# Performance work log

Hardware: AMD Instinct MI355X
Metric: run time of the kernel (lower is better)

Reference implementation:

```python
import jax, jax.numpy as jnp
import numpy as np

B, S, D_MODEL = 2, 2048, 2048
H, HKV, HD = 16, 16, 128


def setup_inputs() -> dict:
    key = jax.random.key(0)
    k1, k2, k3, k4, k5 = jax.random.split(key, 5)
    hidden_states = jax.random.normal(k1, (B, S, D_MODEL), dtype=jnp.float32)
    cos = jax.random.uniform(k2, (S, HD), dtype=jnp.float32)
    sin = jax.random.uniform(k3, (S, HD), dtype=jnp.float32)
    W_qkv = jax.random.normal(k4, (D_MODEL, (H + 2 * HKV) * HD), dtype=jnp.float32) * (D_MODEL ** -0.5)
    W_o = jax.random.normal(k5, (H * HD, D_MODEL), dtype=jnp.float32) * ((H * HD) ** -0.5)
    return {"hidden_states": hidden_states, "cos": cos, "sin": sin, "W_qkv": W_qkv, "W_o": W_o}


def _rotate_half(x):
    x1, x2 = jnp.split(x, 2, axis=-1)
    return jnp.concatenate([-x2, x1], axis=-1)


def reference(hidden_states, cos, sin, W_qkv, W_o):
    b, s, _ = hidden_states.shape
    qkv = jnp.einsum('bsd,de->bse', hidden_states, W_qkv)
    qkv = qkv.reshape(b, s, H + 2 * HKV, HD)  # B S (H+2Hkv) D
    q = qkv[:, :, :H]
    k = qkv[:, :, H:H + HKV]
    v = qkv[:, :, H + HKV:]
    # rotary: cos/sin [S, D] broadcast over batch and heads
    c = cos[None, :, None, :]
    sn = sin[None, :, None, :]
    q = q * c + _rotate_half(q) * sn
    k = k * c + _rotate_half(k) * sn
    # B S H D -> B H S D
    q = jnp.transpose(q, (0, 2, 1, 3))
    k = jnp.transpose(k, (0, 2, 1, 3))
    v = jnp.transpose(v, (0, 2, 1, 3))
    scale = HD ** -0.5
    scores = jnp.einsum('bhqd,bhkd->bhqk', q, k) * scale
    attn = jax.nn.softmax(scores.astype(jnp.float32), axis=-1).astype(q.dtype)
    attn = jax.lax.stop_gradient(attn)  # frozen attention pattern (detach)
    out = jnp.einsum('bhqk,bhkd->bhqd', attn, v)
    out = jnp.transpose(out, (0, 2, 1, 3)).reshape(b, s, H * HD)
    return jnp.einsum('bsd,de->bse', out, W_o)
```

## Files before the change

kernel.cpp:

```cpp
#include <hip/hip_runtime.h>

typedef _Float16 f16;
typedef _Float16 half8 __attribute__((ext_vector_type(8)));
typedef _Float16 half4 __attribute__((ext_vector_type(4)));
typedef float f32x4 __attribute__((ext_vector_type(4)));

#define B_ 2
#define S_ 2048
#define DM_ 2048
#define H_ 16
#define HD_ 128
#define EQ_ 6144
#define SCALE_Q 0.08838834764831845f
#define DEFER_THR 8.0f

__device__ __forceinline__ void gload16(const void* g, void* l) {
  __builtin_amdgcn_global_load_lds(
      (const __attribute__((address_space(1))) unsigned int*)g,
      (__attribute__((address_space(3))) unsigned int*)l, 16, 0, 0);
}

__device__ __forceinline__ float red16_max(float x) {
  float t;
  t = __builtin_bit_cast(float, __builtin_amdgcn_mov_dpp(__builtin_bit_cast(int, x), 0xB1, 0xF, 0xF, true));
  x = fmaxf(x, t);
  t = __builtin_bit_cast(float, __builtin_amdgcn_mov_dpp(__builtin_bit_cast(int, x), 0x4E, 0xF, 0xF, true));
  x = fmaxf(x, t);
  t = __builtin_bit_cast(float, __builtin_amdgcn_mov_dpp(__builtin_bit_cast(int, x), 0x141, 0xF, 0xF, true));
  x = fmaxf(x, t);
  t = __builtin_bit_cast(float, __builtin_amdgcn_mov_dpp(__builtin_bit_cast(int, x), 0x140, 0xF, 0xF, true));
  x = fmaxf(x, t);
  return x;
}
__device__ __forceinline__ float red16_sum(float x) {
  float t;
  t = __builtin_bit_cast(float, __builtin_amdgcn_mov_dpp(__builtin_bit_cast(int, x), 0xB1, 0xF, 0xF, true));
  x += t;
  t = __builtin_bit_cast(float, __builtin_amdgcn_mov_dpp(__builtin_bit_cast(int, x), 0x4E, 0xF, 0xF, true));
  x += t;
  t = __builtin_bit_cast(float, __builtin_amdgcn_mov_dpp(__builtin_bit_cast(int, x), 0x141, 0xF, 0xF, true));
  x += t;
  t = __builtin_bit_cast(float, __builtin_amdgcn_mov_dpp(__builtin_bit_cast(int, x), 0x140, 0xF, 0xF, true));
  x += t;
  return x;
}

__global__ void k_cast(const float* __restrict__ in, f16* __restrict__ out, int n4) {
  int i = blockIdx.x * blockDim.x + threadIdx.x;
  int stride = gridDim.x * blockDim.x;
  for (; i < n4; i += stride) {
    float4 v = ((const float4*)in)[i];
    half4 h = { (f16)v.x, (f16)v.y, (f16)v.z, (f16)v.w };
    ((half4*)out)[i] = h;
  }
}

__global__ void k_tcast(const float* __restrict__ in, f16* __restrict__ out, int K, int N) {
  __shared__ float tile[64][65];
  const int t = threadIdx.x;
  const int nb = blockIdx.x * 64, kb = blockIdx.y * 64;
  const int tr = t >> 4, tc4 = (t & 15) * 4;
  #pragma unroll
  for (int i = 0; i < 4; ++i) {
    int k = tr + i * 16;
    float4 v = *(const float4*)&in[(size_t)(kb + k) * N + nb + tc4];
    tile[k][tc4 + 0] = v.x; tile[k][tc4 + 1] = v.y;
    tile[k][tc4 + 2] = v.z; tile[k][tc4 + 3] = v.w;
  }
  __syncthreads();
  #pragma unroll
  for (int i = 0; i < 4; ++i) {
    int n = tr + i * 16;
    half4 h = { (f16)tile[tc4 + 0][n], (f16)tile[tc4 + 1][n],
                (f16)tile[tc4 + 2][n], (f16)tile[tc4 + 3][n] };
    *(half4*)&out[(size_t)(nb + n) * K + kb + tc4] = h;
  }
}

__global__ __launch_bounds__(256, 2) void k_gemm(
    const f16* __restrict__ A, const f16* __restrict__ Bt,
    f16* __restrict__ C16, float* __restrict__ C32,
    int M, int N, int K, int writeF32)
{
  __shared__ __attribute__((aligned(16))) f16 As[2 * 128 * 64];
  __shared__ __attribute__((aligned(16))) f16 Bs[2 * 128 * 64];
  const int t = threadIdx.x;
  const int lane = t & 63, wave = t >> 6;
  const int lr = lane & 15, hi4 = lane >> 4;
  const int wr = wave >> 1, wc = wave & 1;
  const int row0 = blockIdx.x * 128, col0 = blockIdx.y * 128;

  const int srow = lane >> 3, schunk = lane & 7;
  const f16* gA = &A[(size_t)(row0 + wave * 32 + srow) * K + ((schunk ^ srow) * 8)];
  const f16* gB = &Bt[(size_t)(col0 + wave * 32 + srow) * K + ((schunk ^ srow) * 8)];
  char* asb = (char*)As;
  char* bsb = (char*)Bs;

  f32x4 acc[4][4];
  #pragma unroll
  for (int m = 0; m < 4; ++m)
    #pragma unroll
    for (int n = 0; n < 4; ++n)
      acc[m][n] = (f32x4){0.f, 0.f, 0.f, 0.f};

  const int nk = K >> 6;
  #pragma unroll
  for (int i = 0; i < 4; ++i) {
    gload16(gA + (size_t)(i * 8) * K, asb + wave * 4096 + i * 1024);
    gload16(gB + (size_t)(i * 8) * K, bsb + wave * 4096 + i * 1024);
  }
  __syncthreads();

  int cur = 0;
  for (int kt = 0; kt < nk; ++kt) {
    if (kt + 1 < nk) {
      int nb = cur ^ 1;
      #pragma unroll
      for (int i = 0; i < 4; ++i) {
        gload16(gA + (size_t)(i * 8) * K + (kt + 1) * 64, asb + nb * 16384 + wave * 4096 + i * 1024);
        gload16(gB + (size_t)(i * 8) * K + (kt + 1) * 64, bsb + nb * 16384 + wave * 4096 + i * 1024);
      }
    }
    const char* ab = asb + cur * 16384;
    const char* bb = bsb + cur * 16384;
    #pragma unroll
    for (int ks = 0; ks < 2; ++ks) {
      half8 af[4], bf[4];
      #pragma unroll
      for (int m = 0; m < 4; ++m) {
        int ar = wr * 64 + m * 16 + lr;
        af[m] = *(const half8*)(ab + ar * 128 + (((ks * 4 + hi4) ^ (ar & 7)) << 4));
      }
      #pragma unroll
      for (int n = 0; n < 4; ++n) {
        int br = wc * 64 + n * 16 + lr;
        bf[n] = *(const half8*)(bb + br * 128 + (((ks * 4 + hi4) ^ (br & 7)) << 4));
      }
      #pragma unroll
      for (int m = 0; m < 4; ++m)
        #pragma unroll
        for (int n = 0; n < 4; ++n)
          acc[m][n] = __builtin_amdgcn_mfma_f32_16x16x32_f16(af[m], bf[n], acc[m][n], 0, 0, 0);
    }
    __syncthreads();
    cur ^= 1;
  }
  #pragma unroll
  for (int m = 0; m < 4; ++m)
    #pragma unroll
    for (int n = 0; n < 4; ++n)
      #pragma unroll
      for (int j = 0; j < 4; ++j) {
        int row = row0 + wr * 64 + m * 16 + hi4 * 4 + j;
        int col = col0 + wc * 64 + n * 16 + lr;
        if (writeF32) C32[(size_t)row * N + col] = acc[m][n][j];
        else          C16[(size_t)row * N + col] = (f16)acc[m][n][j];
      }
  (void)M;
}

__global__ void k_rope(const f16* __restrict__ qkv, const float* __restrict__ cosb,
                       const float* __restrict__ sinb, f16* __restrict__ Qf, f16* __restrict__ Kf)
{
  const int bx = blockIdx.x;
  const int bs = bx >> 4;
  const int h = (bx & 15) * 2 + (threadIdx.x >> 7);
  const int d = threadIdx.x & 127;
  const int s = bs & (S_ - 1);
  const int b = bs >> 11;
  float x  = (float)qkv[(size_t)bs * EQ_ + h * HD_ + d];
  float xp = (float)qkv[(size_t)bs * EQ_ + h * HD_ + (d ^ 64)];
  float sgn = (d < 64) ? -1.0f : 1.0f;
  float v = x * cosb[s * HD_ + d] + sgn * xp * sinb[s * HD_ + d];
  if (h < H_) {
    v *= SCALE_Q;
    Qf[(((size_t)(b * H_ + h)) * S_ + s) * HD_ + d] = (f16)v;
  } else {
    Kf[(((size_t)(b * H_ + (h - H_))) * S_ + s) * HD_ + d] = (f16)v;
  }
}

__global__ void k_vtrans(const f16* __restrict__ qkv, f16* __restrict__ VT)
{
  __shared__ __attribute__((aligned(16))) f16 tile[128][136];
  const int bx = blockIdx.x;
  const int st = bx & 15, h = (bx >> 4) & 15, b = bx >> 8;
  const int t = threadIdx.x;
  const int sl = t >> 1, dc = (t & 1) * 64;
  const int bs = b * S_ + st * 128 + sl;
  #pragma unroll
  for (int i = 0; i < 8; ++i) {
    half8 v = *(const half8*)&qkv[(size_t)bs * EQ_ + (32 + h) * HD_ + dc + i * 8];
    *(half8*)&tile[sl][dc + i * 8] = v;
  }
  __syncthreads();
  const int dr = t >> 1, scc = (t & 1) * 64;
  #pragma unroll
  for (int i = 0; i < 8; ++i) {
    half8 v;
    #pragma unroll
    for (int j = 0; j < 8; ++j) v[j] = tile[scc + i * 8 + j][dr];
    *(half8*)&VT[(((size_t)(b * H_ + h)) * HD_ + dr) * S_ + st * 128 + scc + i * 8] = v;
  }
}

__global__ __launch_bounds__(256, 2) void k_attn(
    const f16* __restrict__ Qf, const f16* __restrict__ Kf, const f16* __restrict__ VT,
    f16* __restrict__ Oout)
{
  __shared__ __attribute__((aligned(16))) char lds[32768];
  char* Ks = lds;
  char* Vs = lds + 16384;
  const int bx = blockIdx.x;
  const int hg = bx & 31, qt = bx >> 5;
  const int h = hg & 15, b = hg >> 4;
  const int t = threadIdx.x, lane = t & 63, wave = t >> 6;
  const int lr = lane & 15, hi4 = lane >> 4;
  char* Ps = Ks + wave * 4096;
  const size_t bh = (size_t)(b * H_ + h);
  const int q0 = qt * 128 + wave * 32;

  half8 qf[2][4];
  #pragma unroll
  for (int m = 0; m < 2; ++m)
    #pragma unroll
    for (int ds = 0; ds < 4; ++ds)
      qf[m][ds] = *(const half8*)&Qf[(bh * S_ + q0 + m * 16 + lr) * HD_ + ds * 32 + hi4 * 8];

  f32x4 o[2][8];
  #pragma unroll
  for (int m = 0; m < 2; ++m)
    #pragma unroll
    for (int dc = 0; dc < 8; ++dc) o[m][dc] = (f32x4){0.f, 0.f, 0.f, 0.f};
  float mstate[2][4], lstate[2][4];
  #pragma unroll
  for (int m = 0; m < 2; ++m)
    #pragma unroll
    for (int j = 0; j < 4; ++j) { mstate[m][j] = -1e30f; lstate[m][j] = 0.f; }

  const f16* Kg = &Kf[bh * S_ * HD_];
  const f16* Vg = &VT[bh * HD_ * S_];

  for (int kt = 0; kt < S_ / 64; ++kt) {
    __syncthreads();
    #pragma unroll
    for (int i = 0; i < 4; ++i) {
      int row = wave * 16 + i * 4 + (lane >> 4);
      int ch  = (lane & 15) ^ (row & 7);
      gload16(Kg + (size_t)(kt * 64 + row) * HD_ + ch * 8, Ks + wave * 4096 + i * 1024);
    }
    #pragma unroll
    for (int i = 0; i < 4; ++i) {
      int d  = wave * 32 + i * 8 + (lane >> 3);
      int ch = (lane & 7) ^ (d & 7);
      gload16(Vg + (size_t)d * S_ + kt * 64 + ch * 8, Vs + wave * 4096 + i * 1024);
    }
    asm volatile("s_waitcnt vmcnt(4)" ::: "memory");
    __builtin_amdgcn_s_barrier();
    __builtin_amdgcn_sched_barrier(0);

    f32x4 sc[2][4];
    #pragma unroll
    for (int m = 0; m < 2; ++m)
      #pragma unroll
      for (int n = 0; n < 4; ++n) sc[m][n] = (f32x4){0.f, 0.f, 0.f, 0.f};
    #pragma unroll
    for (int ds = 0; ds < 4; ++ds) {
      half8 kf[4];
      #pragma unroll
      for (int n = 0; n < 4; ++n) {
        int ar = n * 16 + lr;
        kf[n] = *(const half8*)(Ks + ar * 256 + ((((ds * 4 + hi4) ^ (ar & 7))) << 4));
      }
      #pragma unroll
      for (int m = 0; m < 2; ++m)
        #pragma unroll
        for (int n = 0; n < 4; ++n)
          sc[m][n] = __builtin_amdgcn_mfma_f32_16x16x32_f16(qf[m][ds], kf[n], sc[m][n], 0, 0, 0);
    }
    __syncthreads();

    float mx[2][4];
    #pragma unroll
    for (int m = 0; m < 2; ++m)
      #pragma unroll
      for (int j = 0; j < 4; ++j) {
        mx[m][j] = fmaxf(fmaxf(sc[m][0][j], sc[m][1][j]), fmaxf(sc[m][2][j], sc[m][3][j]));
        mx[m][j] = red16_max(mx[m][j]);
      }
    float dmax = -1e30f;
    #pragma unroll
    for (int m = 0; m < 2; ++m)
      #pragma unroll
      for (int j = 0; j < 4; ++j)
        dmax = fmaxf(dmax, mx[m][j] - mstate[m][j]);
    if (__any(dmax > DEFER_THR)) {
      #pragma unroll
      for (int m = 0; m < 2; ++m)
        #pragma unroll
        for (int j = 0; j < 4; ++j) {
          float nm = fmaxf(mstate[m][j], mx[m][j]);
          float corr = __expf(mstate[m][j] - nm);
          mstate[m][j] = nm;
          lstate[m][j] *= corr;
          #pragma unroll
          for (int dc = 0; dc < 8; ++dc) o[m][dc][j] *= corr;
        }
    }
    float rs[2][4];
    #pragma unroll
    for (int m = 0; m < 2; ++m)
      #pragma unroll
      for (int j = 0; j < 4; ++j) rs[m][j] = 0.f;
    #pragma unroll
    for (int m = 0; m < 2; ++m)
      #pragma unroll
      for (int n = 0; n < 4; ++n)
        #pragma unroll
        for (int j = 0; j < 4; ++j) {
          float p = __expf(sc[m][n][j] - mstate[m][j]);
          sc[m][n][j] = p;
          rs[m][j] += p;
        }
    #pragma unroll
    for (int m = 0; m < 2; ++m)
      #pragma unroll
      for (int j = 0; j < 4; ++j)
        lstate[m][j] += red16_sum(rs[m][j]);

    #pragma unroll
    for (int m = 0; m < 2; ++m)
      #pragma unroll
      for (int n = 0; n < 4; ++n)
        #pragma unroll
        for (int j = 0; j < 4; ++j) {
          int prow = m * 16 + hi4 * 4 + j;
          *(f16*)(Ps + prow * 128 + ((n * 32 + lr * 2) ^ ((prow & 7) << 4))) = (f16)sc[m][n][j];
        }
    asm volatile("" ::: "memory");

    #pragma unroll
    for (int ks = 0; ks < 2; ++ks) {
      half8 pa[2];
      #pragma unroll
      for (int m = 0; m < 2; ++m) {
        int pr = m * 16 + lr;
        pa[m] = *(const half8*)(Ps + pr * 128 + ((((ks * 4 + hi4) ^ (pr & 7))) << 4));
      }
      #pragma unroll
      for (int dc = 0; dc < 8; ++dc) {
        int rv = dc * 16 + lr;
        half8 vb = *(const half8*)(Vs + rv * 128 + ((((ks * 4 + hi4) ^ (rv & 7))) << 4));
        #pragma unroll
        for (int m = 0; m < 2; ++m)
          o[m][dc] = __builtin_amdgcn_mfma_f32_16x16x32_f16(pa[m], vb, o[m][dc], 0, 0, 0);
      }
    }
  }

  float inv[2][4];
  #pragma unroll
  for (int m = 0; m < 2; ++m)
    #pragma unroll
    for (int j = 0; j < 4; ++j) inv[m][j] = 1.0f / lstate[m][j];
  #pragma unroll
  for (int m = 0; m < 2; ++m)
    #pragma unroll
    for (int dc = 0; dc < 8; ++dc)
      #pragma unroll
      for (int j = 0; j < 4; ++j) {
        int row = b * S_ + qt * 128 + wave * 32 + m * 16 + hi4 * 4 + j;
        int col = h * 128 + dc * 16 + lr;
        Oout[(size_t)row * DM_ + col] = (f16)(o[m][dc][j] * inv[m][j]);
      }
}

extern "C" void kernel_launch(void* const* d_in, const int* in_sizes, int n_in,
                              void* d_out, int out_size, void* d_ws, size_t ws_size,
                              hipStream_t stream) {
  (void)in_sizes; (void)n_in; (void)out_size; (void)ws_size;
  const float* hidden = (const float*)d_in[0];
  const float* cosb   = (const float*)d_in[1];
  const float* sinb   = (const float*)d_in[2];
  const float* W_qkv  = (const float*)d_in[3];
  const float* W_o    = (const float*)d_in[4];
  float* out = (float*)d_out;

  f16* Ah    = (f16*)d_ws;
  f16* Wqt   = Ah    + (size_t)8388608;
  f16* Wot   = Wqt   + (size_t)12582912;
  f16* qkv16 = Wot   + (size_t)4194304;
  f16* Qf    = qkv16 + (size_t)25165824;
  f16* Kf    = Qf    + (size_t)8388608;
  f16* VT    = Kf    + (size_t)8388608;
  f16* AO    = VT    + (size_t)8388608;

  k_cast<<<2048, 256, 0, stream>>>(hidden, Ah, 2097152);
  k_tcast<<<dim3(EQ_ / 64, 2048 / 64), 256, 0, stream>>>(W_qkv, Wqt, 2048, EQ_);
  k_tcast<<<dim3(2048 / 64, 2048 / 64), 256, 0, stream>>>(W_o, Wot, 2048, 2048);
  k_gemm<<<dim3(32, EQ_ / 128), 256, 0, stream>>>(Ah, Wqt, qkv16, nullptr, 4096, EQ_, 2048, 0);
  k_rope<<<B_ * S_ * 16, 256, 0, stream>>>(qkv16, cosb, sinb, Qf, Kf);
  k_vtrans<<<512, 256, 0, stream>>>(qkv16, VT);
  k_attn<<<512, 256, 0, stream>>>(Qf, Kf, VT, AO);
  k_gemm<<<dim3(32, 16), 256, 0, stream>>>(AO, Wot, nullptr, out, 4096, 2048, 2048, 1);
}
```

Before: 433.9 us.

## Use 256x256-tile GEMM for QKV projection and vectorize RoPE kernel

Adds a 512-thread GEMM kernel with 256x256 output tiles and double-buffered LDS staging, used for the QKV projection. Each wave computes a 128x64 sub-tile, which raises operand reuse and arithmetic intensity per LDS byte. The grid shrinks to 384 blocks, which may underfill the GPU's CUs and uses more registers. RoPE is also rewritten so each thread processes 8 element pairs with half8 and float4 vector loads, replacing scalar per-element loads.

```diff
diff --git a/kernel.cpp b/kernel.cpp
--- a/kernel.cpp
+++ b/kernel.cpp
@@ -75,6 +75,83 @@
                 (f16)tile[tc4 + 2][n], (f16)tile[tc4 + 3][n] };
     *(half4*)&out[(size_t)(nb + n) * K + kb + tc4] = h;
   }
+}
+
+__global__ __launch_bounds__(512, 2) void k_gemm256(
+    const f16* __restrict__ A, const f16* __restrict__ Bt, f16* __restrict__ C,
+    int N, int K)
+{
+  __shared__ __attribute__((aligned(16))) f16 As[2][256 * 64];
+  __shared__ __attribute__((aligned(16))) f16 Bs[2][256 * 64];
+  const int t = threadIdx.x;
+  const int lane = t & 63, wave = t >> 6;
+  const int lr = lane & 15, hi4 = lane >> 4;
+  const int wm = wave >> 2, wn = wave & 3;
+  const int row0 = blockIdx.x * 256, col0 = blockIdx.y * 256;
+
+  const int srow = lane >> 3, schunk = lane & 7;
+  const f16* gA = &A[(size_t)(row0 + wave * 32 + srow) * K + ((schunk ^ srow) * 8)];
+  const f16* gB = &Bt[(size_t)(col0 + wave * 32 + srow) * K + ((schunk ^ srow) * 8)];
+
+  f32x4 acc[8][4];
+  #pragma unroll
+  for (int m = 0; m < 8; ++m)
+    #pragma unroll
+    for (int n = 0; n < 4; ++n)
+      acc[m][n] = (f32x4){0.f, 0.f, 0.f, 0.f};
+
+  const int nk = K >> 6;
+  #pragma unroll
+  for (int i = 0; i < 4; ++i) {
+    gload16(gA + (size_t)(i * 8) * K, (char*)As[0] + wave * 4096 + i * 1024);
+    gload16(gB + (size_t)(i * 8) * K, (char*)Bs[0] + wave * 4096 + i * 1024);
+  }
+  __syncthreads();
+
+  for (int kt = 0; kt < nk; ++kt) {
+    const int cur = kt & 1;
+    if (kt + 1 < nk) {
+      #pragma unroll
+      for (int i = 0; i < 4; ++i) {
+        gload16(gA + (size_t)(i * 8) * K + (kt + 1) * 64, (char*)As[cur ^ 1] + wave * 4096 + i * 1024);
+        gload16(gB + (size_t)(i * 8) * K + (kt + 1) * 64, (char*)Bs[cur ^ 1] + wave * 4096 + i * 1024);
+      }
+    }
+    const char* ab = (const char*)As[cur];
+    const char* bb = (const char*)Bs[cur];
+    #pragma unroll
+    for (int ks = 0; ks < 2; ++ks) {
+      half8 af[8], bf[4];
+      #pragma unroll
+      for (int m = 0; m < 8; ++m) {
+        int ar = wm * 128 + m * 16 + lr;
+        af[m] = *(const half8*)(ab + ar * 128 + (((ks * 4 + hi4) ^ (ar & 7)) << 4));
+      }
+      #pragma unroll
+      for (int n = 0; n < 4; ++n) {
+        int br = wn * 64 + n * 16 + lr;
+        bf[n] = *(const half8*)(bb + br * 128 + (((ks * 4 + hi4) ^ (br & 7)) << 4));
+      }
+      __builtin_amdgcn_s_setprio(1);
+      #pragma unroll
+      for (int m = 0; m < 8; ++m)
+        #pragma unroll
+        for (int n = 0; n < 4; ++n)
+          acc[m][n] = __builtin_amdgcn_mfma_f32_16x16x32_f16(af[m], bf[n], acc[m][n], 0, 0, 0);
+      __builtin_amdgcn_s_setprio(0);
+    }
+    __syncthreads();
+  }
+  #pragma unroll
+  for (int m = 0; m < 8; ++m)
+    #pragma unroll
+    for (int n = 0; n < 4; ++n)
+      #pragma unroll
+      for (int j = 0; j < 4; ++j) {
+        int row = row0 + wm * 128 + m * 16 + hi4 * 4 + j;
+        int col = col0 + wn * 64 + n * 16 + lr;
+        C[(size_t)row * N + col] = (f16)acc[m][n][j];
+      }
 }
 
 __global__ __launch_bounds__(256, 2) void k_gemm(
@@ -162,22 +239,33 @@
 __global__ void k_rope(const f16* __restrict__ qkv, const float* __restrict__ cosb,
                        const float* __restrict__ sinb, f16* __restrict__ Qf, f16* __restrict__ Kf)
 {
-  const int bx = blockIdx.x;
-  const int bs = bx >> 4;
-  const int h = (bx & 15) * 2 + (threadIdx.x >> 7);
-  const int d = threadIdx.x & 127;
-  const int s = bs & (S_ - 1);
-  const int b = bs >> 11;
-  float x  = (float)qkv[(size_t)bs * EQ_ + h * HD_ + d];
-  float xp = (float)qkv[(size_t)bs * EQ_ + h * HD_ + (d ^ 64)];
-  float sgn = (d < 64) ? -1.0f : 1.0f;
-  float v = x * cosb[s * HD_ + d] + sgn * xp * sinb[s * HD_ + d];
-  if (h < H_) {
-    v *= SCALE_Q;
-    Qf[(((size_t)(b * H_ + h)) * S_ + s) * HD_ + d] = (f16)v;
-  } else {
-    Kf[(((size_t)(b * H_ + (h - H_))) * S_ + s) * HD_ + d] = (f16)v;
-  }
+  const int idx = blockIdx.x * 256 + threadIdx.x;
+  const int oct = idx & 7;
+  const int h = (idx >> 3) & 31;
+  const int bs = idx >> 8;
+  const int s = bs & (S_ - 1), b = bs >> 11;
+  const f16* base = qkv + (size_t)bs * EQ_ + h * HD_;
+  half8 lo = *(const half8*)(base + oct * 8);
+  half8 hi = *(const half8*)(base + 64 + oct * 8);
+  const float* cl = cosb + s * HD_ + oct * 8;
+  const float* sl = sinb + s * HD_ + oct * 8;
+  float c[8], cu[8], sn[8], su[8];
+  ((float4*)c)[0]  = *(const float4*)(cl);      ((float4*)c)[1]  = *(const float4*)(cl + 4);
+  ((float4*)cu)[0] = *(const float4*)(cl + 64); ((float4*)cu)[1] = *(const float4*)(cl + 68);
+  ((float4*)sn)[0] = *(const float4*)(sl);      ((float4*)sn)[1] = *(const float4*)(sl + 4);
+  ((float4*)su)[0] = *(const float4*)(sl + 64); ((float4*)su)[1] = *(const float4*)(sl + 68);
+  const float scale = (h < H_) ? SCALE_Q : 1.0f;
+  half8 olo, ohi;
+  #pragma unroll
+  for (int j = 0; j < 8; ++j) {
+    float x = (float)lo[j], xp = (float)hi[j];
+    olo[j] = (f16)((x * c[j] - xp * sn[j]) * scale);
+    ohi[j] = (f16)((xp * cu[j] + x * su[j]) * scale);
+  }
+  f16* dst = (h < H_) ? Qf : Kf;
+  const size_t off = ((size_t)(b * H_ + (h & 15)) * S_ + s) * HD_;
+  *(half8*)(dst + off + oct * 8) = olo;
+  *(half8*)(dst + off + 64 + oct * 8) = ohi;
 }
 
 __global__ void k_vtrans(const f16* __restrict__ qkv, f16* __restrict__ VT)
@@ -398,8 +486,8 @@
   k_cast<<<2048, 256, 0, stream>>>(hidden, Ah, 2097152);
   k_tcast<<<dim3(EQ_ / 64, 2048 / 64), 256, 0, stream>>>(W_qkv, Wqt, 2048, EQ_);
   k_tcast<<<dim3(2048 / 64, 2048 / 64), 256, 0, stream>>>(W_o, Wot, 2048, 2048);
-  k_gemm<<<dim3(32, EQ_ / 128), 256, 0, stream>>>(Ah, Wqt, qkv16, nullptr, 4096, EQ_, 2048, 0);
-  k_rope<<<B_ * S_ * 16, 256, 0, stream>>>(qkv16, cosb, sinb, Qf, Kf);
+  k_gemm256<<<dim3(16, 24), 512, 0, stream>>>(Ah, Wqt, qkv16, EQ_, 2048);
+  k_rope<<<4096, 256, 0, stream>>>(qkv16, cosb, sinb, Qf, Kf);
   k_vtrans<<<512, 256, 0, stream>>>(qkv16, VT);
   k_attn<<<512, 256, 0, stream>>>(Qf, Kf, VT, AO);
   k_gemm<<<dim3(32, 16), 256, 0, stream>>>(AO, Wot, nullptr, out, 4096, 2048, 2048, 1);
```

New measurement: 441.5 us. Within noise of the previous version (+1.7%).
